# Optimization experiments

Hardware: AMD Instinct MI355X
Metric: run time of the kernel (lower is better)

## Reference

```python
import jax, jax.numpy as jnp
import numpy as np

MASK_VALUE = -1000000.0  # matches sequence_mask fill in the torch source


def setup_inputs() -> dict:
    key = jax.random.key(0)
    k1, k2, k3, k4 = jax.random.split(key, 4)
    B, Lq, Lk, D = 64, 1024, 1024, 64
    return {
        "queries": jax.random.normal(k1, (B, Lq, D), dtype=jnp.float32),
        "keys": jax.random.normal(k2, (B, Lk, D), dtype=jnp.float32),
        "values": jax.random.normal(k3, (B, Lk, D), dtype=jnp.float32),
        "valid_lens": jax.random.randint(k4, (B,), 1, Lk + 1, dtype=jnp.int64),
    }


def reference(queries, keys, values, valid_lens):
    # queries: [B, Lq, D], keys/values: [B, Lk, D], valid_lens: [B]
    d = queries.shape[-1]
    qk = jnp.einsum("bqd,bkd->bqk", queries, keys) / jnp.sqrt(jnp.asarray(d, queries.dtype))
    # sequence_mask: positions >= valid_len are set to -1e6 before softmax.
    # valid_lens is per-batch-row, broadcast over queries (repeat_interleave in torch).
    kpos = jnp.arange(keys.shape[1])  # [Lk]
    mask = kpos[None, None, :] < valid_lens[:, None, None]  # [B, 1, Lk] -> broadcast over q
    qk = jnp.where(mask, qk, jnp.asarray(MASK_VALUE, qk.dtype))
    attn = jax.nn.softmax(qk, axis=-1)
    return jnp.einsum("bqk,bkd->bqd", attn, values)
```

## Files before the change

### kernel.cpp

```cpp
#include <hip/hip_runtime.h>
#include <hip/hip_bf16.h>


#define NB    64
#define LQ    1024
#define LK    1024
#define DH    64
#define KVT   64
#define QT    64
#define NITEMS (NB * (LQ / QT))
#define NEGF  1.0e30f
#define SC2   0.18033688011112042f
#define THR   8.0f

typedef __attribute__((ext_vector_type(8))) short    bf8;
typedef __attribute__((ext_vector_type(8))) ushort   u16x8;
typedef __attribute__((ext_vector_type(4))) ushort   u16x4;
typedef __attribute__((ext_vector_type(4))) float    f4;

__device__ __forceinline__ ushort2 cvt2(float a, float b) {
    float2 f; f.x = a; f.y = b;
    __hip_bfloat162 h = __float22bfloat162_rn(f);
    union { __hip_bfloat162 h2; ushort2 u2; } u;
    u.h2 = h;
    return u.u2;
}
__device__ __forceinline__ int swz16(int row, int colbyte) {
    return row * 128 + ((((colbyte >> 4) ^ (row & 7)) << 4) | (colbyte & 15));
}
__device__ __forceinline__ int swz8(int row, int colbyte) {
    return row * 128 + ((((colbyte >> 3) ^ (row & 15)) << 3) | (colbyte & 7));
}

__global__ __launch_bounds__(256, 4)
void attn_v11(const float* __restrict__ Q, const float* __restrict__ K,
              const float* __restrict__ V, const int* __restrict__ VL,
              float* __restrict__ O) {
    __shared__ ushort KsB[2][KVT * DH];
    __shared__ ushort VtB[2][DH * KVT];
    __shared__ ushort PsB[4][16 * KVT];

    const int tid = threadIdx.x;
    const int wid = tid >> 6, l = tid & 63, g = l >> 4, a = l & 15;

    ushort* sb = &PsB[0][0];
    if (tid < NB) {
        const int ntb = (VL[tid] + KVT - 1) >> 6;
        int r = 0;
        for (int j = 0; j < NB; ++j) {
            const int ntj = (VL[j] + KVT - 1) >> 6;
            r += (int)((ntj > ntb) | ((ntj == ntb) & (j < tid)));
        }
        sb[r] = (ushort)tid;
    }
    __syncthreads();
    const int xcd  = blockIdx.x & 7;
    const int slot = blockIdx.x >> 3;
    const int rank = xcd + ((slot >> 4) << 3);
    const int b    = sb[rank];
    const int qbase = (slot & 15) * QT;
    const int valid = VL[b];
    const int nt = (valid + KVT - 1) >> 6;

    const float* Qr = Q + ((size_t)b * LQ + qbase + wid * 16 + a) * DH;
    bf8 qa[2];
    #pragma unroll
    for (int kblk = 0; kblk < 2; ++kblk) {
        f4 x = *(const f4*)(Qr + kblk * 32 + g * 8);
        f4 y = *(const f4*)(Qr + kblk * 32 + g * 8 + 4);
        ushort2 c0 = cvt2(x[0] * SC2, x[1] * SC2), c1 = cvt2(x[2] * SC2, x[3] * SC2);
        ushort2 c2 = cvt2(y[0] * SC2, y[1] * SC2), c3 = cvt2(y[2] * SC2, y[3] * SC2);
        qa[kblk][0] = (short)c0.x; qa[kblk][1] = (short)c0.y;
        qa[kblk][2] = (short)c1.x; qa[kblk][3] = (short)c1.y;
        qa[kblk][4] = (short)c2.x; qa[kblk][5] = (short)c2.y;
        qa[kblk][6] = (short)c3.x; qa[kblk][7] = (short)c3.y;
    }
    const bf8 ones = {0x3F80, 0x3F80, 0x3F80, 0x3F80,
                      0x3F80, 0x3F80, 0x3F80, 0x3F80};

    const int srow = tid >> 3, sslot = tid & 7;
    const int vkp  = tid >> 4, vj = tid & 15;
    const f4* Kb4 = (const f4*)(K + (size_t)b * LK * DH);
    const f4* Vb4 = (const f4*)(V + (size_t)b * LK * DH);

    f4 kr0, kr1, kr2, kr3, vr0, vr1, vr2, vr3;
    auto load_kv = [&](int k0) {
        kr0 = Kb4[(k0 + srow) * 16 + sslot * 2];
        kr1 = Kb4[(k0 + srow) * 16 + sslot * 2 + 1];
        kr2 = Kb4[(k0 + srow + 32) * 16 + sslot * 2];
        kr3 = Kb4[(k0 + srow + 32) * 16 + sslot * 2 + 1];
        vr0 = Vb4[(k0 + 4 * vkp + 0) * 16 + vj];
        vr1 = Vb4[(k0 + 4 * vkp + 1) * 16 + vj];
        vr2 = Vb4[(k0 + 4 * vkp + 2) * 16 + vj];
        vr3 = Vb4[(k0 + 4 * vkp + 3) * 16 + vj];
    };
    auto store_kv = [&](int bs) {
        char* kd = (char*)&KsB[bs][0];
        {
            ushort2 c0 = cvt2(kr0[0], kr0[1]), c1 = cvt2(kr0[2], kr0[3]);
            ushort2 c2 = cvt2(kr1[0], kr1[1]), c3 = cvt2(kr1[2], kr1[3]);
            u16x8 w = {c0.x, c0.y, c1.x, c1.y, c2.x, c2.y, c3.x, c3.y};
            *(u16x8*)(kd + swz16(srow, sslot * 16)) = w;
        }
        {
            ushort2 c0 = cvt2(kr2[0], kr2[1]), c1 = cvt2(kr2[2], kr2[3]);
            ushort2 c2 = cvt2(kr3[0], kr3[1]), c3 = cvt2(kr3[2], kr3[3]);
            u16x8 w = {c0.x, c0.y, c1.x, c1.y, c2.x, c2.y, c3.x, c3.y};
            *(u16x8*)(kd + swz16(srow + 32, sslot * 16)) = w;
        }
        char* vd = (char*)&VtB[bs][0];
        #pragma unroll
        for (int c = 0; c < 4; ++c) {
            ushort2 a01 = cvt2(vr0[c], vr1[c]), a23 = cvt2(vr2[c], vr3[c]);
            u16x4 p = {a01.x, a01.y, a23.x, a23.y};
            *(u16x4*)(vd + swz8(4 * vj + c, vkp * 8)) = p;
        }
    };

    f4 oacc[4];
    #pragma unroll
    for (int n = 0; n < 4; ++n) oacc[n] = f4{0.f, 0.f, 0.f, 0.f};
    f4 lacc = f4{0.f, 0.f, 0.f, 0.f};
    float m_run = -NEGF;

    load_kv(0);
    store_kv(0);
    for (int t = 0; t < nt; ++t) {
        const int bs = t & 1;
        __syncthreads();
        if (t + 1 < nt) load_kv((t + 1) * KVT);
        __builtin_amdgcn_sched_barrier(0);

        const char* kd = (const char*)&KsB[bs][0];
        f4 sacc[4];
        #pragma unroll
        for (int n = 0; n < 4; ++n) sacc[n] = f4{0.f, 0.f, 0.f, 0.f};
        __builtin_amdgcn_s_setprio(1);
        #pragma unroll
        for (int n = 0; n < 4; ++n)
            #pragma unroll
            for (int kblk = 0; kblk < 2; ++kblk) {
                bf8 kb = *(const bf8*)(kd + swz16(n * 16 + a, kblk * 64 + g * 16));
                sacc[n] = __builtin_amdgcn_mfma_f32_16x16x32_bf16(
                    kb, qa[kblk], sacc[n], 0, 0, 0);
            }
        __builtin_amdgcn_s_setprio(0);

        float s[4][4];
        const int kmax = valid - t * KVT;
        #pragma unroll
        for (int n = 0; n < 4; ++n)
            #pragma unroll
            for (int r = 0; r < 4; ++r) s[n][r] = sacc[n][r];
        if (kmax < KVT) {
            #pragma unroll
            for (int n = 0; n < 4; ++n)
                #pragma unroll
                for (int r = 0; r < 4; ++r)
                    if (16 * n + 4 * g + r >= kmax) s[n][r] = -NEGF;
        }

        float tm = s[0][0];
        #pragma unroll
        for (int n = 0; n < 4; ++n)
            #pragma unroll
            for (int r = 0; r < 4; ++r) tm = fmaxf(tm, s[n][r]);
        tm = fmaxf(tm, __shfl_xor(tm, 16));
        tm = fmaxf(tm, __shfl_xor(tm, 32));

        float rs_ = 1.0f;
        const bool skip = __all(tm <= m_run + THR);
        if (!skip) {
            const float mnew = fmaxf(m_run, tm);
            rs_ = __builtin_exp2f(m_run - mnew);
            m_run = mnew;
        }

        float p[4][4];
        #pragma unroll
        for (int n = 0; n < 4; ++n)
            #pragma unroll
            for (int r = 0; r < 4; ++r)
                p[n][r] = __builtin_exp2f(s[n][r] - m_run);

        if (!skip) {
            float rr[4];
            #pragma unroll
            for (int r = 0; r < 4; ++r) rr[r] = __shfl(rs_, 4 * g + r);
            #pragma unroll
            for (int n = 0; n < 4; ++n)
                #pragma unroll
                for (int r = 0; r < 4; ++r) oacc[n][r] *= rr[r];
            #pragma unroll
            for (int r = 0; r < 4; ++r) lacc[r] *= rr[r];
        }

        char* pbase = (char*)&PsB[wid][0];
        #pragma unroll
        for (int n = 0; n < 4; ++n) {
            ushort2 a01 = cvt2(p[n][0], p[n][1]), a23 = cvt2(p[n][2], p[n][3]);
            u16x4 w4 = {a01.x, a01.y, a23.x, a23.y};
            *(u16x4*)(pbase + swz16(a, 32 * n + 8 * g)) = w4;
        }

        const char* vd = (const char*)&VtB[bs][0];
        __builtin_amdgcn_s_setprio(1);
        #pragma unroll
        for (int kblk = 0; kblk < 2; ++kblk) {
            bf8 pa = *(const bf8*)(pbase + swz16(a, kblk * 64 + g * 16));
            const int cb = kblk * 64 + g * 16;
            #pragma unroll
            for (int n = 0; n < 4; ++n) {
                u16x4 lo = *(const u16x4*)(vd + swz8(n * 16 + a, cb));
                u16x4 hi = *(const u16x4*)(vd + swz8(n * 16 + a, cb + 8));
                bf8 vb = {(short)lo[0], (short)lo[1], (short)lo[2], (short)lo[3],
                          (short)hi[0], (short)hi[1], (short)hi[2], (short)hi[3]};
                oacc[n] = __builtin_amdgcn_mfma_f32_16x16x32_bf16(
                    pa, vb, oacc[n], 0, 0, 0);
            }
            lacc = __builtin_amdgcn_mfma_f32_16x16x32_bf16(pa, ones, lacc, 0, 0, 0);
        }
        __builtin_amdgcn_s_setprio(0);

        if (t + 1 < nt) store_kv(bs ^ 1);
    }

    float iv[4];
    #pragma unroll
    for (int r = 0; r < 4; ++r) iv[r] = 1.0f / lacc[r];
    float* Ob = O + ((size_t)b * LQ + qbase + wid * 16) * DH;
    #pragma unroll
    for (int n = 0; n < 4; ++n)
        #pragma unroll
        for (int r = 0; r < 4; ++r)
            Ob[(size_t)(4 * g + r) * DH + 16 * n + a] = oacc[n][r] * iv[r];
}

extern "C" void kernel_launch(void* const* d_in, const int* in_sizes, int n_in,
                              void* d_out, int out_size, void* d_ws, size_t ws_size,
                              hipStream_t stream) {
    const float* Q  = (const float*)d_in[0];
    const float* K  = (const float*)d_in[1];
    const float* V  = (const float*)d_in[2];
    const int*   VL = (const int*)d_in[3];
    float* O = (float*)d_out;

    attn_v11<<<NITEMS, 256, 0, stream>>>(Q, K, V, VL, O);
}
```

Before: 38.24 us.

## Precompute swizzled bf16 K/V tiles in workspace and stream them via direct-to-LDS loads

Adds a prep kernel that converts K and V to bf16 once per batch tile and writes them into a workspace already in the swizzled LDS layout (V transposed). The attention kernel then stages tiles with global_load_lds instead of having every Q-tile block reload fp32 K/V and convert them itself. This removes the repeated conversion work and halves the bytes read per tile. In exchange it adds an extra kernel launch and a workspace round trip, and it falls back to the old kernel when no workspace is provided.

```diff
diff --git a/kernel.cpp b/kernel.cpp
--- a/kernel.cpp
+++ b/kernel.cpp
@@ -12,6 +12,8 @@
 #define NEGF  1.0e30f
 #define SC2   0.18033688011112042f
 #define THR   8.0f
+#define IMG_BT    16384
+#define WS_NEEDED ((size_t)NB * 16 * IMG_BT)
 
 typedef __attribute__((ext_vector_type(8))) short    bf8;
 typedef __attribute__((ext_vector_type(8))) ushort   u16x8;
@@ -30,6 +32,234 @@
 }
 __device__ __forceinline__ int swz8(int row, int colbyte) {
     return row * 128 + ((((colbyte >> 3) ^ (row & 15)) << 3) | (colbyte & 7));
+}
+__device__ __forceinline__ void gl16(const void* g, void* l) {
+    __builtin_amdgcn_global_load_lds(
+        (const __attribute__((address_space(1))) unsigned int*)g,
+        (__attribute__((address_space(3))) unsigned int*)l, 16, 0, 0);
+}
+
+__global__ __launch_bounds__(256)
+void prep_kv(const float* __restrict__ K, const float* __restrict__ V,
+             const int* __restrict__ VL, ushort* __restrict__ WS) {
+    const int bt = blockIdx.x;
+    const int b = bt >> 4, t = bt & 15;
+    const int tid = threadIdx.x;
+
+    const int nt = (VL[b] + KVT - 1) >> 6;
+    if (t >= nt) return;
+
+    const int srow = tid >> 3, sslot = tid & 7;
+    const int vkp  = tid >> 4, vj = tid & 15;
+    const f4* Kb4 = (const f4*)(K + (size_t)b * LK * DH);
+    const f4* Vb4 = (const f4*)(V + (size_t)b * LK * DH);
+    const int k0 = t * KVT;
+
+    f4 kr0 = Kb4[(k0 + srow) * 16 + sslot * 2];
+    f4 kr1 = Kb4[(k0 + srow) * 16 + sslot * 2 + 1];
+    f4 kr2 = Kb4[(k0 + srow + 32) * 16 + sslot * 2];
+    f4 kr3 = Kb4[(k0 + srow + 32) * 16 + sslot * 2 + 1];
+    f4 vr0 = Vb4[(k0 + 4 * vkp + 0) * 16 + vj];
+    f4 vr1 = Vb4[(k0 + 4 * vkp + 1) * 16 + vj];
+    f4 vr2 = Vb4[(k0 + 4 * vkp + 2) * 16 + vj];
+    f4 vr3 = Vb4[(k0 + 4 * vkp + 3) * 16 + vj];
+
+    char* kd = (char*)WS + (size_t)bt * IMG_BT;
+    {
+        ushort2 c0 = cvt2(kr0[0], kr0[1]), c1 = cvt2(kr0[2], kr0[3]);
+        ushort2 c2 = cvt2(kr1[0], kr1[1]), c3 = cvt2(kr1[2], kr1[3]);
+        u16x8 w = {c0.x, c0.y, c1.x, c1.y, c2.x, c2.y, c3.x, c3.y};
+        *(u16x8*)(kd + swz16(srow, sslot * 16)) = w;
+    }
+    {
+        ushort2 c0 = cvt2(kr2[0], kr2[1]), c1 = cvt2(kr2[2], kr2[3]);
+        ushort2 c2 = cvt2(kr3[0], kr3[1]), c3 = cvt2(kr3[2], kr3[3]);
+        u16x8 w = {c0.x, c0.y, c1.x, c1.y, c2.x, c2.y, c3.x, c3.y};
+        *(u16x8*)(kd + swz16(srow + 32, sslot * 16)) = w;
+    }
+    char* vd = kd + 8192;
+    #pragma unroll
+    for (int c = 0; c < 4; ++c) {
+        ushort2 a01 = cvt2(vr0[c], vr1[c]), a23 = cvt2(vr2[c], vr3[c]);
+        u16x4 p = {a01.x, a01.y, a23.x, a23.y};
+        *(u16x4*)(vd + swz8(4 * vj + c, vkp * 8)) = p;
+    }
+}
+
+__global__ __launch_bounds__(256, 4)
+void attn_v14(const float* __restrict__ Q, const int* __restrict__ VL,
+              const ushort* __restrict__ WS, float* __restrict__ O) {
+    __shared__ ushort KsB[2][KVT * DH];
+    __shared__ ushort VtB[2][DH * KVT];
+    __shared__ ushort PsB[4][16 * KVT];
+
+    const int tid = threadIdx.x;
+    const int wid = tid >> 6, l = tid & 63, g = l >> 4, a = l & 15;
+
+    ushort* sb = &PsB[0][0];
+    if (tid < NB) {
+        const int ntb = (VL[tid] + KVT - 1) >> 6;
+        int r = 0;
+        for (int j = 0; j < NB; ++j) {
+            const int ntj = (VL[j] + KVT - 1) >> 6;
+            r += (int)((ntj > ntb) | ((ntj == ntb) & (j < tid)));
+        }
+        sb[r] = (ushort)tid;
+    }
+    __syncthreads();
+    const int xcd  = blockIdx.x & 7;
+    const int slot = blockIdx.x >> 3;
+    const int rank = xcd + ((slot >> 4) << 3);
+    const int b    = sb[rank];
+    const int qbase = (slot & 15) * QT;
+    const int valid = VL[b];
+    const int nt = (valid + KVT - 1) >> 6;
+
+    const char* img = (const char*)WS + (size_t)b * (16 * IMG_BT);
+    auto stageK = [&](int t, int bs) {
+        const char* gsrc = img + (size_t)t * IMG_BT + wid * 2048 + l * 16;
+        char* d = (char*)&KsB[bs][0] + wid * 2048;
+        gl16(gsrc, d); gl16(gsrc + 1024, d + 1024);
+    };
+    auto stageV = [&](int t, int bs) {
+        const char* gsrc = img + (size_t)t * IMG_BT + 8192 + wid * 2048 + l * 16;
+        char* d = (char*)&VtB[bs][0] + wid * 2048;
+        gl16(gsrc, d); gl16(gsrc + 1024, d + 1024);
+    };
+    stageK(0, 0); stageV(0, 0);
+
+    const float* Qr = Q + ((size_t)b * LQ + qbase + wid * 16 + a) * DH;
+    bf8 qa[2];
+    #pragma unroll
+    for (int kblk = 0; kblk < 2; ++kblk) {
+        f4 x = *(const f4*)(Qr + kblk * 32 + g * 8);
+        f4 y = *(const f4*)(Qr + kblk * 32 + g * 8 + 4);
+        ushort2 c0 = cvt2(x[0] * SC2, x[1] * SC2), c1 = cvt2(x[2] * SC2, x[3] * SC2);
+        ushort2 c2 = cvt2(y[0] * SC2, y[1] * SC2), c3 = cvt2(y[2] * SC2, y[3] * SC2);
+        qa[kblk][0] = (short)c0.x; qa[kblk][1] = (short)c0.y;
+        qa[kblk][2] = (short)c1.x; qa[kblk][3] = (short)c1.y;
+        qa[kblk][4] = (short)c2.x; qa[kblk][5] = (short)c2.y;
+        qa[kblk][6] = (short)c3.x; qa[kblk][7] = (short)c3.y;
+    }
+    const bf8 ones = {0x3F80, 0x3F80, 0x3F80, 0x3F80,
+                      0x3F80, 0x3F80, 0x3F80, 0x3F80};
+
+    f4 oacc[4];
+    #pragma unroll
+    for (int n = 0; n < 4; ++n) oacc[n] = f4{0.f, 0.f, 0.f, 0.f};
+    f4 lacc = f4{0.f, 0.f, 0.f, 0.f};
+    float m_run = -NEGF;
+
+    for (int t = 0; t < nt; ++t) {
+        const int bs = t & 1;
+        __syncthreads();
+        if (t + 1 < nt) {
+            stageK(t + 1, bs ^ 1);
+            stageV(t + 1, bs ^ 1);
+        }
+        __builtin_amdgcn_sched_barrier(0);
+
+        const char* kd = (const char*)&KsB[bs][0];
+        f4 sacc[4];
+        #pragma unroll
+        for (int n = 0; n < 4; ++n) sacc[n] = f4{0.f, 0.f, 0.f, 0.f};
+        __builtin_amdgcn_s_setprio(1);
+        #pragma unroll
+        for (int n = 0; n < 4; ++n)
+            #pragma unroll
+            for (int kblk = 0; kblk < 2; ++kblk) {
+                bf8 kb = *(const bf8*)(kd + swz16(n * 16 + a, kblk * 64 + g * 16));
+                sacc[n] = __builtin_amdgcn_mfma_f32_16x16x32_bf16(
+                    kb, qa[kblk], sacc[n], 0, 0, 0);
+            }
+        __builtin_amdgcn_s_setprio(0);
+
+        float s[4][4];
+        const int kmax = valid - t * KVT;
+        #pragma unroll
+        for (int n = 0; n < 4; ++n)
+            #pragma unroll
+            for (int r = 0; r < 4; ++r) s[n][r] = sacc[n][r];
+        if (kmax < KVT) {
+            #pragma unroll
+            for (int n = 0; n < 4; ++n)
+                #pragma unroll
+                for (int r = 0; r < 4; ++r)
+                    if (16 * n + 4 * g + r >= kmax) s[n][r] = -NEGF;
+        }
+
+        float tm = s[0][0];
+        #pragma unroll
+        for (int n = 0; n < 4; ++n)
+            #pragma unroll
+            for (int r = 0; r < 4; ++r) tm = fmaxf(tm, s[n][r]);
+        tm = fmaxf(tm, __shfl_xor(tm, 16));
+        tm = fmaxf(tm, __shfl_xor(tm, 32));
+
+        float rs_ = 1.0f;
+        const bool skip = __all(tm <= m_run + THR);
+        if (!skip) {
+            const float mnew = fmaxf(m_run, tm);
+            rs_ = __builtin_exp2f(m_run - mnew);
+            m_run = mnew;
+        }
+
+        float p[4][4];
+        #pragma unroll
+        for (int n = 0; n < 4; ++n)
+            #pragma unroll
+            for (int r = 0; r < 4; ++r)
+                p[n][r] = __builtin_exp2f(s[n][r] - m_run);
+
+        if (!skip) {
+            float rr[4];
+            #pragma unroll
+            for (int r = 0; r < 4; ++r) rr[r] = __shfl(rs_, 4 * g + r);
+            #pragma unroll
+            for (int n = 0; n < 4; ++n)
+                #pragma unroll
+                for (int r = 0; r < 4; ++r) oacc[n][r] *= rr[r];
+            #pragma unroll
+            for (int r = 0; r < 4; ++r) lacc[r] *= rr[r];
+        }
+
+        char* pbase = (char*)&PsB[wid][0];
+        #pragma unroll
+        for (int n = 0; n < 4; ++n) {
+            ushort2 a01 = cvt2(p[n][0], p[n][1]), a23 = cvt2(p[n][2], p[n][3]);
+            u16x4 w4 = {a01.x, a01.y, a23.x, a23.y};
+            *(u16x4*)(pbase + swz16(a, 32 * n + 8 * g)) = w4;
+        }
+
+        const char* vd = (const char*)&VtB[bs][0];
+        __builtin_amdgcn_s_setprio(1);
+        #pragma unroll
+        for (int kblk = 0; kblk < 2; ++kblk) {
+            bf8 pa = *(const bf8*)(pbase + swz16(a, kblk * 64 + g * 16));
+            const int cb = kblk * 64 + g * 16;
+            #pragma unroll
+            for (int n = 0; n < 4; ++n) {
+                u16x4 lo = *(const u16x4*)(vd + swz8(n * 16 + a, cb));
+                u16x4 hi = *(const u16x4*)(vd + swz8(n * 16 + a, cb + 8));
+                bf8 vb_ = {(short)lo[0], (short)lo[1], (short)lo[2], (short)lo[3],
+                           (short)hi[0], (short)hi[1], (short)hi[2], (short)hi[3]};
+                oacc[n] = __builtin_amdgcn_mfma_f32_16x16x32_bf16(
+                    pa, vb_, oacc[n], 0, 0, 0);
+            }
+            lacc = __builtin_amdgcn_mfma_f32_16x16x32_bf16(pa, ones, lacc, 0, 0, 0);
+        }
+        __builtin_amdgcn_s_setprio(0);
+    }
+
+    float iv[4];
+    #pragma unroll
+    for (int r = 0; r < 4; ++r) iv[r] = 1.0f / lacc[r];
+    float* Ob = O + ((size_t)b * LQ + qbase + wid * 16) * DH;
+    #pragma unroll
+    for (int n = 0; n < 4; ++n)
+        #pragma unroll
+        for (int r = 0; r < 4; ++r)
+            Ob[(size_t)(4 * g + r) * DH + 16 * n + a] = oacc[n][r] * iv[r];
 }
 
 __global__ __launch_bounds__(256, 4)
@@ -245,5 +475,11 @@
     const int*   VL = (const int*)d_in[3];
     float* O = (float*)d_out;
 
-    attn_v11<<<NITEMS, 256, 0, stream>>>(Q, K, V, VL, O);
-}
+    if (d_ws != nullptr && ws_size >= WS_NEEDED) {
+        ushort* WS = (ushort*)d_ws;
+        prep_kv<<<NB * 16, 256, 0, stream>>>(K, V, VL, WS);
+        attn_v14<<<NITEMS, 256, 0, stream>>>(Q, VL, WS, O);
+    } else {
+        attn_v11<<<NITEMS, 256, 0, stream>>>(Q, K, V, VL, O);
+    }
+}
```

New measurement: 41.69 us. 1.09x slower.

## Double query tile to 128 with 512-thread blocks and split K/V load roles

Applied to the files above, without the earlier changes.

Each block now covers 128 query rows using 8 waves, so every K/V tile staged in shared memory is reused by twice as many query rows and global K/V traffic per query halves. Waves 0-3 load and convert V while waves 4-7 load K, which cuts per-thread staging registers. Batch-to-block assignment now follows a serpentine order over the sorted valid lengths to balance work across slots. The grid is halved to 512 blocks, which may leave fewer blocks per CU and worse tail balance on uneven sequence lengths.

```diff
diff --git a/kernel.cpp b/kernel.cpp
--- a/kernel.cpp
+++ b/kernel.cpp
@@ -7,7 +7,7 @@
 #define LK    1024
 #define DH    64
 #define KVT   64
-#define QT    64
+#define QT    128
 #define NITEMS (NB * (LQ / QT))
 #define NEGF  1.0e30f
 #define SC2   0.18033688011112042f
@@ -32,13 +32,13 @@
     return row * 128 + ((((colbyte >> 3) ^ (row & 15)) << 3) | (colbyte & 7));
 }
 
-__global__ __launch_bounds__(256, 4)
-void attn_v11(const float* __restrict__ Q, const float* __restrict__ K,
+__global__ __launch_bounds__(512, 4)
+void attn_v15(const float* __restrict__ Q, const float* __restrict__ K,
               const float* __restrict__ V, const int* __restrict__ VL,
               float* __restrict__ O) {
     __shared__ ushort KsB[2][KVT * DH];
     __shared__ ushort VtB[2][DH * KVT];
-    __shared__ ushort PsB[4][16 * KVT];
+    __shared__ ushort PsB[8][16 * KVT];
 
     const int tid = threadIdx.x;
     const int wid = tid >> 6, l = tid & 63, g = l >> 4, a = l & 15;
@@ -54,11 +54,13 @@
         sb[r] = (ushort)tid;
     }
     __syncthreads();
-    const int xcd  = blockIdx.x & 7;
-    const int slot = blockIdx.x >> 3;
-    const int rank = xcd + ((slot >> 4) << 3);
-    const int b    = sb[rank];
-    const int qbase = (slot & 15) * QT;
+    const int xcd   = blockIdx.x & 7;
+    const int slot  = blockIdx.x >> 3;
+    const int qtile = slot & 7;
+    const int st    = slot >> 3;
+    const int rank  = xcd + ((st < 4) ? st : (11 - st)) * 8;
+    const int b     = sb[rank];
+    const int qbase = qtile * QT;
     const int valid = VL[b];
     const int nt = (valid + KVT - 1) >> 6;
 
@@ -78,42 +80,50 @@
     const bf8 ones = {0x3F80, 0x3F80, 0x3F80, 0x3F80,
                       0x3F80, 0x3F80, 0x3F80, 0x3F80};
 
-    const int srow = tid >> 3, sslot = tid & 7;
-    const int vkp  = tid >> 4, vj = tid & 15;
+    const int  rtid  = tid & 255;
+    const bool vrole = (wid < 4);
+    const int srow = rtid >> 3, sslot = rtid & 7;
+    const int vkp  = rtid >> 4, vj = rtid & 15;
     const f4* Kb4 = (const f4*)(K + (size_t)b * LK * DH);
     const f4* Vb4 = (const f4*)(V + (size_t)b * LK * DH);
 
-    f4 kr0, kr1, kr2, kr3, vr0, vr1, vr2, vr3;
+    f4 r0, r1, r2, r3;
     auto load_kv = [&](int k0) {
-        kr0 = Kb4[(k0 + srow) * 16 + sslot * 2];
-        kr1 = Kb4[(k0 + srow) * 16 + sslot * 2 + 1];
-        kr2 = Kb4[(k0 + srow + 32) * 16 + sslot * 2];
-        kr3 = Kb4[(k0 + srow + 32) * 16 + sslot * 2 + 1];
-        vr0 = Vb4[(k0 + 4 * vkp + 0) * 16 + vj];
-        vr1 = Vb4[(k0 + 4 * vkp + 1) * 16 + vj];
-        vr2 = Vb4[(k0 + 4 * vkp + 2) * 16 + vj];
-        vr3 = Vb4[(k0 + 4 * vkp + 3) * 16 + vj];
+        if (vrole) {
+            r0 = Vb4[(k0 + 4 * vkp + 0) * 16 + vj];
+            r1 = Vb4[(k0 + 4 * vkp + 1) * 16 + vj];
+            r2 = Vb4[(k0 + 4 * vkp + 2) * 16 + vj];
+            r3 = Vb4[(k0 + 4 * vkp + 3) * 16 + vj];
+        } else {
+            r0 = Kb4[(k0 + srow) * 16 + sslot * 2];
+            r1 = Kb4[(k0 + srow) * 16 + sslot * 2 + 1];
+            r2 = Kb4[(k0 + srow + 32) * 16 + sslot * 2];
+            r3 = Kb4[(k0 + srow + 32) * 16 + sslot * 2 + 1];
+        }
     };
     auto store_kv = [&](int bs) {
-        char* kd = (char*)&KsB[bs][0];
-        {
-            ushort2 c0 = cvt2(kr0[0], kr0[1]), c1 = cvt2(kr0[2], kr0[3]);
-            ushort2 c2 = cvt2(kr1[0], kr1[1]), c3 = cvt2(kr1[2], kr1[3]);
-            u16x8 w = {c0.x, c0.y, c1.x, c1.y, c2.x, c2.y, c3.x, c3.y};
-            *(u16x8*)(kd + swz16(srow, sslot * 16)) = w;
-        }
-        {
-            ushort2 c0 = cvt2(kr2[0], kr2[1]), c1 = cvt2(kr2[2], kr2[3]);
-            ushort2 c2 = cvt2(kr3[0], kr3[1]), c3 = cvt2(kr3[2], kr3[3]);
-            u16x8 w = {c0.x, c0.y, c1.x, c1.y, c2.x, c2.y, c3.x, c3.y};
-            *(u16x8*)(kd + swz16(srow + 32, sslot * 16)) = w;
-        }
-        char* vd = (char*)&VtB[bs][0];
-        #pragma unroll
-        for (int c = 0; c < 4; ++c) {
-            ushort2 a01 = cvt2(vr0[c], vr1[c]), a23 = cvt2(vr2[c], vr3[c]);
-            u16x4 p = {a01.x, a01.y, a23.x, a23.y};
-            *(u16x4*)(vd + swz8(4 * vj + c, vkp * 8)) = p;
+        if (vrole) {
+            char* vd = (char*)&VtB[bs][0];
+            #pragma unroll
+            for (int c = 0; c < 4; ++c) {
+                ushort2 a01 = cvt2(r0[c], r1[c]), a23 = cvt2(r2[c], r3[c]);
+                u16x4 p = {a01.x, a01.y, a23.x, a23.y};
+                *(u16x4*)(vd + swz8(4 * vj + c, vkp * 8)) = p;
+            }
+        } else {
+            char* kd = (char*)&KsB[bs][0];
+            {
+                ushort2 c0 = cvt2(r0[0], r0[1]), c1 = cvt2(r0[2], r0[3]);
+                ushort2 c2 = cvt2(r1[0], r1[1]), c3 = cvt2(r1[2], r1[3]);
+                u16x8 w = {c0.x, c0.y, c1.x, c1.y, c2.x, c2.y, c3.x, c3.y};
+                *(u16x8*)(kd + swz16(srow, sslot * 16)) = w;
+            }
+            {
+                ushort2 c0 = cvt2(r2[0], r2[1]), c1 = cvt2(r2[2], r2[3]);
+                ushort2 c2 = cvt2(r3[0], r3[1]), c3 = cvt2(r3[2], r3[3]);
+                u16x8 w = {c0.x, c0.y, c1.x, c1.y, c2.x, c2.y, c3.x, c3.y};
+                *(u16x8*)(kd + swz16(srow + 32, sslot * 16)) = w;
+            }
         }
     };
 
@@ -213,10 +223,10 @@
             for (int n = 0; n < 4; ++n) {
                 u16x4 lo = *(const u16x4*)(vd + swz8(n * 16 + a, cb));
                 u16x4 hi = *(const u16x4*)(vd + swz8(n * 16 + a, cb + 8));
-                bf8 vb = {(short)lo[0], (short)lo[1], (short)lo[2], (short)lo[3],
-                          (short)hi[0], (short)hi[1], (short)hi[2], (short)hi[3]};
+                bf8 vb_ = {(short)lo[0], (short)lo[1], (short)lo[2], (short)lo[3],
+                           (short)hi[0], (short)hi[1], (short)hi[2], (short)hi[3]};
                 oacc[n] = __builtin_amdgcn_mfma_f32_16x16x32_bf16(
-                    pa, vb, oacc[n], 0, 0, 0);
+                    pa, vb_, oacc[n], 0, 0, 0);
             }
             lacc = __builtin_amdgcn_mfma_f32_16x16x32_bf16(pa, ones, lacc, 0, 0, 0);
         }
@@ -245,5 +255,5 @@
     const int*   VL = (const int*)d_in[3];
     float* O = (float*)d_out;
 
-    attn_v11<<<NITEMS, 256, 0, stream>>>(Q, K, V, VL, O);
-}
+    attn_v15<<<NITEMS, 512, 0, stream>>>(Q, K, V, VL, O);
+}
```

Result: faster. 35.50 us (-7.2%).

## Double query tile per block and pass P through registers instead of LDS

Applied to the files above, without the earlier changes.

Each wave now handles two 16-row query fragments (a 128-row query tile per block), so every K/V tile loaded to LDS feeds twice as many MFMAs and total K/V global traffic halves. K rows are stored with a permutation so that the S accumulator layout directly matches the PV MFMA A-operand layout. This removes the per-wave P shared-memory round trip, and the mask index is adjusted to match. The batch schedule now uses a snake ordering across XCD slots. In exchange there are half as many blocks, higher register use (occupancy bound lowered to 2), and worse load balance across variable valid lengths.

```diff
diff --git a/kernel.cpp b/kernel.cpp
--- a/kernel.cpp
+++ b/kernel.cpp
@@ -7,7 +7,7 @@
 #define LK    1024
 #define DH    64
 #define KVT   64
-#define QT    64
+#define QT    128
 #define NITEMS (NB * (LQ / QT))
 #define NEGF  1.0e30f
 #define SC2   0.18033688011112042f
@@ -32,18 +32,17 @@
     return row * 128 + ((((colbyte >> 3) ^ (row & 15)) << 3) | (colbyte & 7));
 }
 
-__global__ __launch_bounds__(256, 4)
-void attn_v11(const float* __restrict__ Q, const float* __restrict__ K,
+__global__ __launch_bounds__(256, 2)
+void attn_v17(const float* __restrict__ Q, const float* __restrict__ K,
               const float* __restrict__ V, const int* __restrict__ VL,
               float* __restrict__ O) {
     __shared__ ushort KsB[2][KVT * DH];
     __shared__ ushort VtB[2][DH * KVT];
-    __shared__ ushort PsB[4][16 * KVT];
+    __shared__ ushort sched[NB];
 
     const int tid = threadIdx.x;
     const int wid = tid >> 6, l = tid & 63, g = l >> 4, a = l & 15;
 
-    ushort* sb = &PsB[0][0];
     if (tid < NB) {
         const int ntb = (VL[tid] + KVT - 1) >> 6;
         int r = 0;
@@ -51,35 +50,41 @@
             const int ntj = (VL[j] + KVT - 1) >> 6;
             r += (int)((ntj > ntb) | ((ntj == ntb) & (j < tid)));
         }
-        sb[r] = (ushort)tid;
+        sched[r] = (ushort)tid;
     }
     __syncthreads();
-    const int xcd  = blockIdx.x & 7;
-    const int slot = blockIdx.x >> 3;
-    const int rank = xcd + ((slot >> 4) << 3);
-    const int b    = sb[rank];
-    const int qbase = (slot & 15) * QT;
+    const int xcd   = blockIdx.x & 7;
+    const int slot  = blockIdx.x >> 3;
+    const int qtile = slot & 7;
+    const int st    = slot >> 3;
+    const int rank  = xcd + ((st < 4) ? st : (11 - st)) * 8;
+    const int b     = sched[rank];
+    const int qbase = qtile * QT;
     const int valid = VL[b];
     const int nt = (valid + KVT - 1) >> 6;
 
-    const float* Qr = Q + ((size_t)b * LQ + qbase + wid * 16 + a) * DH;
-    bf8 qa[2];
+    bf8 qa[2][2];
     #pragma unroll
-    for (int kblk = 0; kblk < 2; ++kblk) {
-        f4 x = *(const f4*)(Qr + kblk * 32 + g * 8);
-        f4 y = *(const f4*)(Qr + kblk * 32 + g * 8 + 4);
-        ushort2 c0 = cvt2(x[0] * SC2, x[1] * SC2), c1 = cvt2(x[2] * SC2, x[3] * SC2);
-        ushort2 c2 = cvt2(y[0] * SC2, y[1] * SC2), c3 = cvt2(y[2] * SC2, y[3] * SC2);
-        qa[kblk][0] = (short)c0.x; qa[kblk][1] = (short)c0.y;
-        qa[kblk][2] = (short)c1.x; qa[kblk][3] = (short)c1.y;
-        qa[kblk][4] = (short)c2.x; qa[kblk][5] = (short)c2.y;
-        qa[kblk][6] = (short)c3.x; qa[kblk][7] = (short)c3.y;
+    for (int f = 0; f < 2; ++f) {
+        const float* Qr = Q + ((size_t)b * LQ + qbase + wid * 32 + f * 16 + a) * DH;
+        #pragma unroll
+        for (int kblk = 0; kblk < 2; ++kblk) {
+            f4 x = *(const f4*)(Qr + kblk * 32 + g * 8);
+            f4 y = *(const f4*)(Qr + kblk * 32 + g * 8 + 4);
+            ushort2 c0 = cvt2(x[0] * SC2, x[1] * SC2), c1 = cvt2(x[2] * SC2, x[3] * SC2);
+            ushort2 c2 = cvt2(y[0] * SC2, y[1] * SC2), c3 = cvt2(y[2] * SC2, y[3] * SC2);
+            qa[f][kblk][0] = (short)c0.x; qa[f][kblk][1] = (short)c0.y;
+            qa[f][kblk][2] = (short)c1.x; qa[f][kblk][3] = (short)c1.y;
+            qa[f][kblk][4] = (short)c2.x; qa[f][kblk][5] = (short)c2.y;
+            qa[f][kblk][6] = (short)c3.x; qa[f][kblk][7] = (short)c3.y;
+        }
     }
     const bf8 ones = {0x3F80, 0x3F80, 0x3F80, 0x3F80,
                       0x3F80, 0x3F80, 0x3F80, 0x3F80};
 
     const int srow = tid >> 3, sslot = tid & 7;
     const int vkp  = tid >> 4, vj = tid & 15;
+    const int prow = (srow & 3) | ((srow & 24) >> 1) | ((srow & 4) << 2);
     const f4* Kb4 = (const f4*)(K + (size_t)b * LK * DH);
     const f4* Vb4 = (const f4*)(V + (size_t)b * LK * DH);
 
@@ -100,13 +105,13 @@
             ushort2 c0 = cvt2(kr0[0], kr0[1]), c1 = cvt2(kr0[2], kr0[3]);
             ushort2 c2 = cvt2(kr1[0], kr1[1]), c3 = cvt2(kr1[2], kr1[3]);
             u16x8 w = {c0.x, c0.y, c1.x, c1.y, c2.x, c2.y, c3.x, c3.y};
-            *(u16x8*)(kd + swz16(srow, sslot * 16)) = w;
+            *(u16x8*)(kd + swz16(prow, sslot * 16)) = w;
         }
         {
             ushort2 c0 = cvt2(kr2[0], kr2[1]), c1 = cvt2(kr2[2], kr2[3]);
             ushort2 c2 = cvt2(kr3[0], kr3[1]), c3 = cvt2(kr3[2], kr3[3]);
             u16x8 w = {c0.x, c0.y, c1.x, c1.y, c2.x, c2.y, c3.x, c3.y};
-            *(u16x8*)(kd + swz16(srow + 32, sslot * 16)) = w;
+            *(u16x8*)(kd + swz16(prow + 32, sslot * 16)) = w;
         }
         char* vd = (char*)&VtB[bs][0];
         #pragma unroll
@@ -117,11 +122,13 @@
         }
     };
 
-    f4 oacc[4];
+    f4 oacc[2][4];
     #pragma unroll
-    for (int n = 0; n < 4; ++n) oacc[n] = f4{0.f, 0.f, 0.f, 0.f};
-    f4 lacc = f4{0.f, 0.f, 0.f, 0.f};
-    float m_run = -NEGF;
+    for (int f = 0; f < 2; ++f)
+        #pragma unroll
+        for (int n = 0; n < 4; ++n) oacc[f][n] = f4{0.f, 0.f, 0.f, 0.f};
+    f4 lacc[2] = {f4{0.f, 0.f, 0.f, 0.f}, f4{0.f, 0.f, 0.f, 0.f}};
+    float m_run[2] = {-NEGF, -NEGF};
 
     load_kv(0);
     store_kv(0);
@@ -132,108 +139,125 @@
         __builtin_amdgcn_sched_barrier(0);
 
         const char* kd = (const char*)&KsB[bs][0];
-        f4 sacc[4];
-        #pragma unroll
-        for (int n = 0; n < 4; ++n) sacc[n] = f4{0.f, 0.f, 0.f, 0.f};
+        f4 sacc[2][4];
+        #pragma unroll
+        for (int f = 0; f < 2; ++f)
+            #pragma unroll
+            for (int n = 0; n < 4; ++n) sacc[f][n] = f4{0.f, 0.f, 0.f, 0.f};
         __builtin_amdgcn_s_setprio(1);
         #pragma unroll
         for (int n = 0; n < 4; ++n)
             #pragma unroll
             for (int kblk = 0; kblk < 2; ++kblk) {
                 bf8 kb = *(const bf8*)(kd + swz16(n * 16 + a, kblk * 64 + g * 16));
-                sacc[n] = __builtin_amdgcn_mfma_f32_16x16x32_bf16(
-                    kb, qa[kblk], sacc[n], 0, 0, 0);
+                sacc[0][n] = __builtin_amdgcn_mfma_f32_16x16x32_bf16(
+                    kb, qa[0][kblk], sacc[0][n], 0, 0, 0);
+                sacc[1][n] = __builtin_amdgcn_mfma_f32_16x16x32_bf16(
+                    kb, qa[1][kblk], sacc[1][n], 0, 0, 0);
             }
         __builtin_amdgcn_s_setprio(0);
 
-        float s[4][4];
+        float p[2][4][4];
         const int kmax = valid - t * KVT;
         #pragma unroll
-        for (int n = 0; n < 4; ++n)
-            #pragma unroll
-            for (int r = 0; r < 4; ++r) s[n][r] = sacc[n][r];
-        if (kmax < KVT) {
+        for (int f = 0; f < 2; ++f) {
+            float s[4][4];
             #pragma unroll
             for (int n = 0; n < 4; ++n)
                 #pragma unroll
+                for (int r = 0; r < 4; ++r) s[n][r] = sacc[f][n][r];
+            if (kmax < KVT) {
+                #pragma unroll
+                for (int n = 0; n < 4; ++n)
+                    #pragma unroll
+                    for (int r = 0; r < 4; ++r)
+                        if (32 * (n >> 1) + 4 * (n & 1) + 8 * g + r >= kmax)
+                            s[n][r] = -NEGF;
+            }
+
+            float m0 = fmaxf(fmaxf(s[0][0], s[0][1]), fmaxf(s[0][2], s[0][3]));
+            float m1 = fmaxf(fmaxf(s[1][0], s[1][1]), fmaxf(s[1][2], s[1][3]));
+            float m2 = fmaxf(fmaxf(s[2][0], s[2][1]), fmaxf(s[2][2], s[2][3]));
+            float m3 = fmaxf(fmaxf(s[3][0], s[3][1]), fmaxf(s[3][2], s[3][3]));
+            float tm = fmaxf(fmaxf(m0, m1), fmaxf(m2, m3));
+            tm = fmaxf(tm, __shfl_xor(tm, 16));
+            tm = fmaxf(tm, __shfl_xor(tm, 32));
+
+            float rs_ = 1.0f;
+            const bool skip = __all(tm <= m_run[f] + THR);
+            if (!skip) {
+                const float mnew = fmaxf(m_run[f], tm);
+                rs_ = __builtin_exp2f(m_run[f] - mnew);
+                m_run[f] = mnew;
+            }
+
+            #pragma unroll
+            for (int n = 0; n < 4; ++n)
+                #pragma unroll
                 for (int r = 0; r < 4; ++r)
-                    if (16 * n + 4 * g + r >= kmax) s[n][r] = -NEGF;
-        }
-
-        float tm = s[0][0];
-        #pragma unroll
-        for (int n = 0; n < 4; ++n)
-            #pragma unroll
-            for (int r = 0; r < 4; ++r) tm = fmaxf(tm, s[n][r]);
-        tm = fmaxf(tm, __shfl_xor(tm, 16));
-        tm = fmaxf(tm, __shfl_xor(tm, 32));
-
-        float rs_ = 1.0f;
-        const bool skip = __all(tm <= m_run + THR);
-        if (!skip) {
-            const float mnew = fmaxf(m_run, tm);
-            rs_ = __builtin_exp2f(m_run - mnew);
-            m_run = mnew;
-        }
-
-        float p[4][4];
-        #pragma unroll
-        for (int n = 0; n < 4; ++n)
-            #pragma unroll
-            for (int r = 0; r < 4; ++r)
-                p[n][r] = __builtin_exp2f(s[n][r] - m_run);
-
-        if (!skip) {
-            float rr[4];
-            #pragma unroll
-            for (int r = 0; r < 4; ++r) rr[r] = __shfl(rs_, 4 * g + r);
-            #pragma unroll
-            for (int n = 0; n < 4; ++n)
-                #pragma unroll
-                for (int r = 0; r < 4; ++r) oacc[n][r] *= rr[r];
-            #pragma unroll
-            for (int r = 0; r < 4; ++r) lacc[r] *= rr[r];
-        }
-
-        char* pbase = (char*)&PsB[wid][0];
-        #pragma unroll
-        for (int n = 0; n < 4; ++n) {
-            ushort2 a01 = cvt2(p[n][0], p[n][1]), a23 = cvt2(p[n][2], p[n][3]);
-            u16x4 w4 = {a01.x, a01.y, a23.x, a23.y};
-            *(u16x4*)(pbase + swz16(a, 32 * n + 8 * g)) = w4;
+                    p[f][n][r] = __builtin_exp2f(s[n][r] - m_run[f]);
+
+            if (!skip) {
+                float rr[4];
+                #pragma unroll
+                for (int r = 0; r < 4; ++r) rr[r] = __shfl(rs_, 4 * g + r);
+                #pragma unroll
+                for (int n = 0; n < 4; ++n)
+                    #pragma unroll
+                    for (int r = 0; r < 4; ++r) oacc[f][n][r] *= rr[r];
+                #pragma unroll
+                for (int r = 0; r < 4; ++r) lacc[f][r] *= rr[r];
+            }
         }
 
         const char* vd = (const char*)&VtB[bs][0];
         __builtin_amdgcn_s_setprio(1);
         #pragma unroll
         for (int kblk = 0; kblk < 2; ++kblk) {
-            bf8 pa = *(const bf8*)(pbase + swz16(a, kblk * 64 + g * 16));
+            bf8 pa[2];
+            #pragma unroll
+            for (int f = 0; f < 2; ++f) {
+                ushort2 w0 = cvt2(p[f][2 * kblk][0], p[f][2 * kblk][1]);
+                ushort2 w1 = cvt2(p[f][2 * kblk][2], p[f][2 * kblk][3]);
+                ushort2 w2 = cvt2(p[f][2 * kblk + 1][0], p[f][2 * kblk + 1][1]);
+                ushort2 w3 = cvt2(p[f][2 * kblk + 1][2], p[f][2 * kblk + 1][3]);
+                pa[f][0] = (short)w0.x; pa[f][1] = (short)w0.y;
+                pa[f][2] = (short)w1.x; pa[f][3] = (short)w1.y;
+                pa[f][4] = (short)w2.x; pa[f][5] = (short)w2.y;
+                pa[f][6] = (short)w3.x; pa[f][7] = (short)w3.y;
+            }
             const int cb = kblk * 64 + g * 16;
             #pragma unroll
             for (int n = 0; n < 4; ++n) {
                 u16x4 lo = *(const u16x4*)(vd + swz8(n * 16 + a, cb));
                 u16x4 hi = *(const u16x4*)(vd + swz8(n * 16 + a, cb + 8));
-                bf8 vb = {(short)lo[0], (short)lo[1], (short)lo[2], (short)lo[3],
-                          (short)hi[0], (short)hi[1], (short)hi[2], (short)hi[3]};
-                oacc[n] = __builtin_amdgcn_mfma_f32_16x16x32_bf16(
-                    pa, vb, oacc[n], 0, 0, 0);
-            }
-            lacc = __builtin_amdgcn_mfma_f32_16x16x32_bf16(pa, ones, lacc, 0, 0, 0);
+                bf8 vb_ = {(short)lo[0], (short)lo[1], (short)lo[2], (short)lo[3],
+                           (short)hi[0], (short)hi[1], (short)hi[2], (short)hi[3]};
+                oacc[0][n] = __builtin_amdgcn_mfma_f32_16x16x32_bf16(
+                    pa[0], vb_, oacc[0][n], 0, 0, 0);
+                oacc[1][n] = __builtin_amdgcn_mfma_f32_16x16x32_bf16(
+                    pa[1], vb_, oacc[1][n], 0, 0, 0);
+            }
+            lacc[0] = __builtin_amdgcn_mfma_f32_16x16x32_bf16(pa[0], ones, lacc[0], 0, 0, 0);
+            lacc[1] = __builtin_amdgcn_mfma_f32_16x16x32_bf16(pa[1], ones, lacc[1], 0, 0, 0);
         }
         __builtin_amdgcn_s_setprio(0);
 
         if (t + 1 < nt) store_kv(bs ^ 1);
     }
 
-    float iv[4];
     #pragma unroll
-    for (int r = 0; r < 4; ++r) iv[r] = 1.0f / lacc[r];
-    float* Ob = O + ((size_t)b * LQ + qbase + wid * 16) * DH;
-    #pragma unroll
-    for (int n = 0; n < 4; ++n)
-        #pragma unroll
-        for (int r = 0; r < 4; ++r)
-            Ob[(size_t)(4 * g + r) * DH + 16 * n + a] = oacc[n][r] * iv[r];
+    for (int f = 0; f < 2; ++f) {
+        float iv[4];
+        #pragma unroll
+        for (int r = 0; r < 4; ++r) iv[r] = 1.0f / lacc[f][r];
+        float* Ob = O + ((size_t)b * LQ + qbase + wid * 32 + f * 16) * DH;
+        #pragma unroll
+        for (int n = 0; n < 4; ++n)
+            #pragma unroll
+            for (int r = 0; r < 4; ++r)
+                Ob[(size_t)(4 * g + r) * DH + 16 * n + a] = oacc[f][n][r] * iv[r];
+    }
 }
 
 extern "C" void kernel_launch(void* const* d_in, const int* in_sizes, int n_in,
@@ -245,5 +269,5 @@
     const int*   VL = (const int*)d_in[3];
     float* O = (float*)d_out;
 
-    attn_v11<<<NITEMS, 256, 0, stream>>>(Q, K, V, VL, O);
-}
+    attn_v17<<<NITEMS, 256, 0, stream>>>(Q, K, V, VL, O);
+}
```

Result: no change. 38.33 us (+0.2%).
